# Optimization experiments

Measured on AMD Instinct MI355X. Metric: run time of the kernel, lower is better.

## Reference

```python
import jax, jax.numpy as jnp
import numpy as np

B, S, E, H = 8, 2048, 512, 8
DH = E // H
NEG = -1e30


def setup_inputs() -> dict:
    key = jax.random.key(0)
    ks = jax.random.split(key, 6)
    return {
        "x": jax.random.normal(ks[0], (B, S, E), dtype=jnp.float32),
        "W_qkv": jax.random.normal(ks[1], (E, 3 * E), dtype=jnp.float32) * 0.02,
        "b_qkv": jax.random.normal(ks[2], (3 * E,), dtype=jnp.float32) * 0.02,
        "W_out": jax.random.normal(ks[3], (E, E), dtype=jnp.float32) * 0.02,
        "b_out": jax.random.normal(ks[4], (E,), dtype=jnp.float32) * 0.02,
        "rel_pos": jax.random.normal(ks[5], (1, H, S, S), dtype=jnp.float32) * 0.02,
    }


def reference(x, W_qkv, b_qkv, W_out, b_out, rel_pos):
    b, s, e = x.shape
    scale = DH ** -0.5
    qkv = x @ W_qkv + b_qkv                     # [b, s, 3e]
    qkv = qkv.reshape(b, s, 3, H, DH)
    q = jnp.transpose(qkv[:, :, 0], (0, 2, 1, 3))  # [b, h, s, dh]
    k = jnp.transpose(qkv[:, :, 1], (0, 2, 1, 3))
    v = jnp.transpose(qkv[:, :, 2], (0, 2, 1, 3))
    scores = jnp.einsum("bhqd,bhkd->bhqk", q, k) * scale
    scores = scores + rel_pos[:, :, :s, :s]
    causal = jnp.tril(jnp.ones((s, s), dtype=bool))
    scores = jnp.where(causal[None, None], scores, NEG)
    attn = jax.nn.softmax(scores, axis=-1)
    out = jnp.einsum("bhqk,bhkd->bhqd", attn, v)  # [b, h, s, dh]
    out = jnp.transpose(out, (0, 2, 1, 3)).reshape(b, s, e)
    return out @ W_out + b_out
```

## Files before the change

kernel.cpp:

```cpp
#include <hip/hip_runtime.h>
#include <cstdint>


#define DEVI __device__ __forceinline__

typedef __bf16 bf8 __attribute__((ext_vector_type(8)));
typedef float f4 __attribute__((ext_vector_type(4)));
typedef unsigned short us8 __attribute__((ext_vector_type(8)));
typedef unsigned short us4 __attribute__((ext_vector_type(4)));

typedef const unsigned int __attribute__((address_space(1))) gu32;
typedef unsigned int __attribute__((address_space(3))) lu32;

DEVI unsigned short f2bf(float f) {
  unsigned u = __builtin_bit_cast(unsigned, f);
  u += 0x7fffu + ((u >> 16) & 1u);
  return (unsigned short)(u >> 16);
}

DEVI unsigned short cbf(float f) {
  return __builtin_bit_cast(unsigned short, (__bf16)f);
}

DEVI void gl_lds16(const void* g, void* l) {
  __builtin_amdgcn_global_load_lds((gu32*)g, (lu32*)l, 16, 0, 0);
}

DEVI bf8 comb(us4 a, us4 b) {
  us8 r;
  r[0]=a[0]; r[1]=a[1]; r[2]=a[2]; r[3]=a[3];
  r[4]=b[0]; r[5]=b[1]; r[6]=b[2]; r[7]=b[3];
  return __builtin_bit_cast(bf8, r);
}

__global__ __launch_bounds__(256) void k_convert_x(const float* __restrict__ x,
                                                   unsigned short* __restrict__ xb) {
  int c = blockIdx.x * 256 + threadIdx.x;
  int row = c >> 6, cl = c & 63;
  const float* s = x + ((size_t)row << 9) + (cl << 3);
  float4 a = *(const float4*)s;
  float4 b = *(const float4*)(s + 4);
  us8 o;
  o[0]=f2bf(a.x); o[1]=f2bf(a.y); o[2]=f2bf(a.z); o[3]=f2bf(a.w);
  o[4]=f2bf(b.x); o[5]=f2bf(b.y); o[6]=f2bf(b.z); o[7]=f2bf(b.w);
  int p = (cl & ~7) | ((cl & 7) ^ (row & 7));
  *(us8*)(xb + ((size_t)row << 9) + (p << 3)) = o;
}

__global__ __launch_bounds__(256) void k_transpose_w(const float* __restrict__ W,
                                                     unsigned short* __restrict__ Wt, int N) {
  __shared__ float t[32][33];
  int k0 = blockIdx.x * 32, n0 = blockIdx.y * 32;
  int tx = threadIdx.x & 31, ty = threadIdx.x >> 5;
#pragma unroll
  for (int r = 0; r < 4; ++r)
    t[ty + r * 8][tx] = W[(size_t)(k0 + ty + r * 8) * N + n0 + tx];
  __syncthreads();
#pragma unroll
  for (int r = 0; r < 4; ++r) {
    int n = n0 + ty + r * 8, k = k0 + tx;
    int k2 = (k & ~63) | ((((k >> 3) & 7) ^ (n & 7)) << 3) | (k & 7);
    Wt[((size_t)n << 9) + k2] = f2bf(t[tx][ty + r * 8]);
  }
}

__global__ __launch_bounds__(256) void k_relconv(const float* __restrict__ rel,
                                                 unsigned short* __restrict__ relt) {
  int t = blockIdx.x * 256 + threadIdx.x;
  int lane = t & 63, ct = (t >> 6) & 3, kt = (t >> 8) & 31, q16 = (t >> 13) & 127, h = t >> 20;
  if (kt > (q16 >> 2)) return;
  int row0 = (q16 << 4) + ((lane >> 4) << 2);
  int col = (kt << 6) + (ct << 4) + (lane & 15);
  const float* rp = rel + ((size_t)h << 22) + ((size_t)row0 << 11) + col;
  us4 o;
#pragma unroll
  for (int j = 0; j < 4; ++j) o[j] = f2bf(rp[(size_t)j << 11]);
  size_t idx = ((((((size_t)h << 7) | q16) << 5) | kt) << 2 | ct) << 6 | lane;
  *(us4*)(relt + (idx << 2)) = o;
}

template <int EPI>
__global__ __launch_bounds__(256, 2)
void k_gemm(const unsigned short* __restrict__ Ag, const unsigned short* __restrict__ Bg,
            const float* __restrict__ bias, float* __restrict__ Of,
            unsigned short* __restrict__ Oq, unsigned short* __restrict__ Ok,
            unsigned short* __restrict__ Ov) {
  __shared__ __align__(16) unsigned short lds[128 * 64 * 2];
  unsigned short* Al = lds;
  unsigned short* Bl = lds + 128 * 64;
  const int tid = threadIdx.x, wv = tid >> 6, lane = tid & 63, g = lane >> 4, cl = lane & 15;
  const int wm = wv >> 1, wn = wv & 1;
  const int row0 = blockIdx.x * 128, col0 = blockIdx.y * 128;
  f4 acc[4][4];
#pragma unroll
  for (int i = 0; i < 4; ++i)
#pragma unroll
    for (int j = 0; j < 4; ++j) acc[i][j] = (f4){0.f, 0.f, 0.f, 0.f};

  for (int kt = 0; kt < 8; ++kt) {
#pragma unroll
    for (int j = 0; j < 4; ++j) {
      int ci = wv * 4 + j;
      int gci = ci * 64 + lane;
      int r = gci >> 3, cc = gci & 7;
      gl_lds16(Ag + ((size_t)(row0 + r) << 9) + kt * 64 + cc * 8, Al + ci * 512);
      gl_lds16(Bg + ((size_t)(col0 + r) << 9) + kt * 64 + cc * 8, Bl + ci * 512);
    }
    __syncthreads();
#pragma unroll
    for (int kk = 0; kk < 2; ++kk) {
      bf8 af[4], bb[4];
#pragma unroll
      for (int mf = 0; mf < 4; ++mf) {
        int r = wm * 64 + mf * 16 + cl;
        int cc = (kk * 4 + g) ^ (r & 7);
        af[mf] = *(const bf8*)(Al + r * 64 + cc * 8);
      }
#pragma unroll
      for (int nf = 0; nf < 4; ++nf) {
        int r = wn * 64 + nf * 16 + cl;
        int cc = (kk * 4 + g) ^ (r & 7);
        bb[nf] = *(const bf8*)(Bl + r * 64 + cc * 8);
      }
#pragma unroll
      for (int mf = 0; mf < 4; ++mf)
#pragma unroll
        for (int nf = 0; nf < 4; ++nf)
          acc[mf][nf] = __builtin_amdgcn_mfma_f32_16x16x32_bf16(af[mf], bb[nf], acc[mf][nf], 0, 0, 0);
    }
    __syncthreads();
  }

  if (EPI == 1) {
#pragma unroll
    for (int nf = 0; nf < 4; ++nf) {
      int col = col0 + wn * 64 + nf * 16 + cl;
      float bv = bias[col];
#pragma unroll
      for (int mf = 0; mf < 4; ++mf) {
#pragma unroll
        for (int j = 0; j < 4; ++j) {
          int row = row0 + wm * 64 + mf * 16 + 4 * g + j;
          Of[((size_t)row << 9) + col] = acc[mf][nf][j] + bv;
        }
      }
    }
  } else {
    const int which = col0 >> 9;
#pragma unroll
    for (int nf = 0; nf < 4; ++nf) {
      int col = col0 + wn * 64 + nf * 16 + cl;
      float bv = bias[col];
      int d = col & 63, h = (col >> 6) & 7;
#pragma unroll
      for (int mf = 0; mf < 4; ++mf) {
        int row = row0 + wm * 64 + mf * 16 + 4 * g;
        int b = row >> 11, s = row & 2047;
        size_t fb = ((size_t)b * 8 + h) * 131072;
        if (which == 0) {
#pragma unroll
          for (int j = 0; j < 4; ++j) {
            int ss = s + j;
            size_t off = fb + (size_t)((ss >> 4) * 1024 + (d >> 5) * 512 +
                                       (((d >> 3) & 3) * 16 + (ss & 15)) * 8 + (d & 7));
            Oq[off] = f2bf((acc[mf][nf][j] + bv) * 0.125f);
          }
        } else if (which == 1) {
#pragma unroll
          for (int j = 0; j < 4; ++j) {
            int ss = s + j;
            size_t off = fb + (size_t)((ss >> 6) * 4096 + (d >> 5) * 2048 + ((ss >> 4) & 3) * 512 +
                                       (((d >> 3) & 3) * 16 + (ss & 15)) * 8 + (d & 7));
            Ok[off] = f2bf(acc[mf][nf][j] + bv);
          }
        } else {
          us4 o;
#pragma unroll
          for (int j = 0; j < 4; ++j) o[j] = f2bf(acc[mf][nf][j] + bv);
          size_t off = fb + (size_t)((s >> 6) * 4096 + ((s >> 5) & 1) * 2048 + (d >> 4) * 512 +
                                     ((((s >> 3) & 3) * 16) + (d & 15)) * 8 + (s & 7));
          *(us4*)(Ov + off) = o;
        }
      }
    }
  }
}

template <bool RELT>
__global__ __launch_bounds__(256, 4)
void k_attn(const unsigned short* __restrict__ Qf, const unsigned short* __restrict__ Kf,
            const unsigned short* __restrict__ Vf, const float* __restrict__ rel,
            const unsigned short* __restrict__ relt, unsigned short* __restrict__ AO) {
  __shared__ __align__(16) unsigned short Pl[4][16 * 68];
  const int tid = threadIdx.x, wv = tid >> 6, lane = tid & 63, g = lane >> 4, cl = lane & 15;
  int bid = blockIdx.x;
  int glo = bid & 7, b = (bid >> 3) & 7, chi = bid >> 6;
  int c = chi * 8 + glo;
  int h = c >> 4, i = c & 15;
  size_t fb = (((size_t)b << 3) + h) * 131072;
  const unsigned short* Qp = Qf + fb;
  const unsigned short* Kp = Kf + fb;
  const unsigned short* Vp = Vf + fb;
  const float* relp = rel + ((size_t)h << 22);
  unsigned short* pw = Pl[wv];

  for (int pass = 0; pass < 2; ++pass) {
    const int slab = pass ? (31 - i) : i;
    const int q16 = 4 * slab + wv;
    const int rX = q16 << 4;
    const int ktop = slab;

    bf8 qf[2];
#pragma unroll
    for (int kk = 0; kk < 2; ++kk)
      qf[kk] = *(const bf8*)(Qp + q16 * 1024 + kk * 512 + lane * 8);

    f4 oa[4];
    float mr[4], lr[4];
#pragma unroll
    for (int j = 0; j < 4; ++j) { mr[j] = -1e30f; lr[j] = 0.f; }
#pragma unroll
    for (int ct = 0; ct < 4; ++ct) oa[ct] = (f4){0.f, 0.f, 0.f, 0.f};

    for (int kt = 0; kt <= ktop; ++kt) {
      const int kb = kt << 6;
      const unsigned short* Kt = Kp + kt * 4096;
      const unsigned short* Vt = Vp + kt * 4096;
      bf8 kf[2][4], vf[2][4];
#pragma unroll
      for (int kk = 0; kk < 2; ++kk)
#pragma unroll
        for (int ct = 0; ct < 4; ++ct)
          kf[kk][ct] = *(const bf8*)(Kt + kk * 2048 + ct * 512 + lane * 8);
#pragma unroll
      for (int kk = 0; kk < 2; ++kk)
#pragma unroll
        for (int ct = 0; ct < 4; ++ct)
          vf[kk][ct] = *(const bf8*)(Vt + kk * 2048 + ct * 512 + lane * 8);
      us4 rt4[4];
      float rl[4][4];
      if constexpr (RELT) {
        const unsigned short* tb = relt + (((((size_t)h << 7) | q16) << 5) | kt) * 1024;
#pragma unroll
        for (int ct = 0; ct < 4; ++ct)
          rt4[ct] = *(const us4*)(tb + ((ct << 6) | lane) * 4);
      } else {
        const float* rb = relp + ((size_t)(rX + 4 * g) << 11) + kb + cl;
#pragma unroll
        for (int ct = 0; ct < 4; ++ct)
#pragma unroll
          for (int j = 0; j < 4; ++j) rl[ct][j] = rb[((size_t)j << 11) + ct * 16];
      }
      f4 sa[4];
#pragma unroll
      for (int ct = 0; ct < 4; ++ct) sa[ct] = (f4){0.f, 0.f, 0.f, 0.f};
#pragma unroll
      for (int kk = 0; kk < 2; ++kk)
#pragma unroll
        for (int ct = 0; ct < 4; ++ct)
          sa[ct] = __builtin_amdgcn_mfma_f32_16x16x32_bf16(qf[kk], kf[kk][ct], sa[ct], 0, 0, 0);
      if constexpr (RELT) {
#pragma unroll
        for (int ct = 0; ct < 4; ++ct)
#pragma unroll
          for (int j = 0; j < 4; ++j)
            sa[ct][j] += __builtin_bit_cast(float, (unsigned)rt4[ct][j] << 16);
      } else {
#pragma unroll
        for (int ct = 0; ct < 4; ++ct)
#pragma unroll
          for (int j = 0; j < 4; ++j) sa[ct][j] += rl[ct][j];
      }
      if (kt == ktop) {
#pragma unroll
        for (int ct = 0; ct < 4; ++ct) {
          int kcol = kb + ct * 16 + cl;
#pragma unroll
          for (int j = 0; j < 4; ++j)
            if (kcol > rX + 4 * g + j) sa[ct][j] = -1e30f;
        }
      }
      float al[4];
#pragma unroll
      for (int j = 0; j < 4; ++j) {
        float m0 = fmaxf(fmaxf(sa[0][j], sa[1][j]), fmaxf(sa[2][j], sa[3][j]));
        m0 = fmaxf(m0, __shfl_xor(m0, 1, 16));
        m0 = fmaxf(m0, __shfl_xor(m0, 2, 16));
        m0 = fmaxf(m0, __shfl_xor(m0, 4, 16));
        m0 = fmaxf(m0, __shfl_xor(m0, 8, 16));
        float mn = fmaxf(mr[j], m0);
        al[j] = __expf(mr[j] - mn);
        mr[j] = mn;
      }
#pragma unroll
      for (int ct = 0; ct < 4; ++ct)
#pragma unroll
        for (int j = 0; j < 4; ++j) sa[ct][j] = __expf(sa[ct][j] - mr[j]);
#pragma unroll
      for (int j = 0; j < 4; ++j) {
        float rs = sa[0][j] + sa[1][j] + sa[2][j] + sa[3][j];
        rs += __shfl_xor(rs, 1, 16);
        rs += __shfl_xor(rs, 2, 16);
        rs += __shfl_xor(rs, 4, 16);
        rs += __shfl_xor(rs, 8, 16);
        lr[j] = lr[j] * al[j] + rs;
      }
#pragma unroll
      for (int ct = 0; ct < 4; ++ct) {
        oa[ct][0] *= al[0]; oa[ct][1] *= al[1]; oa[ct][2] *= al[2]; oa[ct][3] *= al[3];
      }
#pragma unroll
      for (int ct = 0; ct < 4; ++ct)
#pragma unroll
        for (int j = 0; j < 4; ++j)
          pw[(4 * g + j) * 68 + ct * 16 + cl] = cbf(sa[ct][j]);
#pragma unroll
      for (int kk = 0; kk < 2; ++kk) {
        us4 p0 = *(const us4*)(pw + cl * 68 + kk * 32 + g * 8);
        us4 p1 = *(const us4*)(pw + cl * 68 + kk * 32 + g * 8 + 4);
        bf8 pf = comb(p0, p1);
#pragma unroll
        for (int ct = 0; ct < 4; ++ct)
          oa[ct] = __builtin_amdgcn_mfma_f32_16x16x32_bf16(pf, vf[kk][ct], oa[ct], 0, 0, 0);
      }
    }
#pragma unroll
    for (int j = 0; j < 4; ++j) {
      float inv = 1.0f / lr[j];
      int s = rX + 4 * g + j;
#pragma unroll
      for (int ct = 0; ct < 4; ++ct) {
        int d = ct * 16 + cl;
        int d2 = (d & 7) | (((d >> 3) ^ (s & 7)) << 3);
        AO[(((size_t)b << 11) + s) * 512 + h * 64 + d2] = cbf(oa[ct][j] * inv);
      }
    }
  }
}

extern "C" void kernel_launch(void* const* d_in, const int* in_sizes, int n_in,
                              void* d_out, int out_size, void* d_ws, size_t ws_size,
                              hipStream_t stream) {
  const float* x    = (const float*)d_in[0];
  const float* Wqkv = (const float*)d_in[1];
  const float* bqkv = (const float*)d_in[2];
  const float* Wout = (const float*)d_in[3];
  const float* bout = (const float*)d_in[4];
  const float* rel  = (const float*)d_in[5];
  float* out = (float*)d_out;

  unsigned short* Qw  = (unsigned short*)d_ws;
  unsigned short* Kw  = Qw  + 8388608;
  unsigned short* Vw  = Kw  + 8388608;
  unsigned short* XA  = Vw  + 8388608;
  unsigned short* WtQ = XA  + 8388608;
  unsigned short* WtO = WtQ + 786432;
  unsigned short* relt= WtO + 262144;
  const bool useT = ws_size >= (34603008ULL + 33554432ULL) * 2ULL;

  k_convert_x<<<dim3(4096), dim3(256), 0, stream>>>(x, XA);
  k_transpose_w<<<dim3(16, 48), dim3(256), 0, stream>>>(Wqkv, WtQ, 1536);
  k_transpose_w<<<dim3(16, 16), dim3(256), 0, stream>>>(Wout, WtO, 512);
  if (useT) k_relconv<<<dim3(32768), dim3(256), 0, stream>>>(rel, relt);
  k_gemm<0><<<dim3(128, 12), dim3(256), 0, stream>>>(XA, WtQ, bqkv, nullptr, Qw, Kw, Vw);
  if (useT) k_attn<true ><<<dim3(1024), dim3(256), 0, stream>>>(Qw, Kw, Vw, rel, relt, XA);
  else      k_attn<false><<<dim3(1024), dim3(256), 0, stream>>>(Qw, Kw, Vw, rel, relt, XA);
  k_gemm<1><<<dim3(128, 4), dim3(256), 0, stream>>>(XA, WtO, bout, out, nullptr, nullptr, nullptr);
}
```

Before: 210.9 us.

## Compute transposed attention tiles so each lane owns one query row

```diff
diff --git a/kernel.cpp b/kernel.cpp
--- a/kernel.cpp
+++ b/kernel.cpp
@@ -24,13 +24,6 @@
 
 DEVI void gl_lds16(const void* g, void* l) {
   __builtin_amdgcn_global_load_lds((gu32*)g, (lu32*)l, 16, 0, 0);
-}
-
-DEVI bf8 comb(us4 a, us4 b) {
-  us8 r;
-  r[0]=a[0]; r[1]=a[1]; r[2]=a[2]; r[3]=a[3];
-  r[4]=b[0]; r[5]=b[1]; r[6]=b[2]; r[7]=b[3];
-  return __builtin_bit_cast(bf8, r);
 }
 
 __global__ __launch_bounds__(256) void k_convert_x(const float* __restrict__ x,
@@ -69,12 +62,11 @@
   int t = blockIdx.x * 256 + threadIdx.x;
   int lane = t & 63, ct = (t >> 6) & 3, kt = (t >> 8) & 31, q16 = (t >> 13) & 127, h = t >> 20;
   if (kt > (q16 >> 2)) return;
-  int row0 = (q16 << 4) + ((lane >> 4) << 2);
-  int col = (kt << 6) + (ct << 4) + (lane & 15);
-  const float* rp = rel + ((size_t)h << 22) + ((size_t)row0 << 11) + col;
+  int row = (q16 << 4) + (lane & 15);
+  int col = (kt << 6) + (ct << 4) + ((lane >> 4) << 2);
+  float4 v = *(const float4*)(rel + ((size_t)h << 22) + ((size_t)row << 11) + col);
   us4 o;
-#pragma unroll
-  for (int j = 0; j < 4; ++j) o[j] = f2bf(rp[(size_t)j << 11]);
+  o[0] = f2bf(v.x); o[1] = f2bf(v.y); o[2] = f2bf(v.z); o[3] = f2bf(v.w);
   size_t idx = ((((((size_t)h << 7) | q16) << 5) | kt) << 2 | ct) << 6 | lane;
   *(us4*)(relt + (idx << 2)) = o;
 }
@@ -191,7 +183,7 @@
 void k_attn(const unsigned short* __restrict__ Qf, const unsigned short* __restrict__ Kf,
             const unsigned short* __restrict__ Vf, const float* __restrict__ rel,
             const unsigned short* __restrict__ relt, unsigned short* __restrict__ AO) {
-  __shared__ __align__(16) unsigned short Pl[4][16 * 68];
+  __shared__ __align__(16) unsigned short Pl[4][16 * 72];
   const int tid = threadIdx.x, wv = tid >> 6, lane = tid & 63, g = lane >> 4, cl = lane & 15;
   int bid = blockIdx.x;
   int glo = bid & 7, b = (bid >> 3) & 7, chi = bid >> 6;
@@ -209,18 +201,17 @@
     const int q16 = 4 * slab + wv;
     const int rX = q16 << 4;
     const int ktop = slab;
+    const int qrow = rX + cl;
 
     bf8 qf[2];
 #pragma unroll
     for (int kk = 0; kk < 2; ++kk)
       qf[kk] = *(const bf8*)(Qp + q16 * 1024 + kk * 512 + lane * 8);
 
-    f4 oa[4];
-    float mr[4], lr[4];
-#pragma unroll
-    for (int j = 0; j < 4; ++j) { mr[j] = -1e30f; lr[j] = 0.f; }
-#pragma unroll
-    for (int ct = 0; ct < 4; ++ct) oa[ct] = (f4){0.f, 0.f, 0.f, 0.f};
+    f4 ot[4];
+    float mr = -1e30f, lr = 0.f;
+#pragma unroll
+    for (int ct = 0; ct < 4; ++ct) ot[ct] = (f4){0.f, 0.f, 0.f, 0.f};
 
     for (int kt = 0; kt <= ktop; ++kt) {
       const int kb = kt << 6;
@@ -238,102 +229,97 @@
         for (int ct = 0; ct < 4; ++ct)
           vf[kk][ct] = *(const bf8*)(Vt + kk * 2048 + ct * 512 + lane * 8);
       us4 rt4[4];
-      float rl[4][4];
+      float4 rl4[4];
       if constexpr (RELT) {
         const unsigned short* tb = relt + (((((size_t)h << 7) | q16) << 5) | kt) * 1024;
 #pragma unroll
         for (int ct = 0; ct < 4; ++ct)
           rt4[ct] = *(const us4*)(tb + ((ct << 6) | lane) * 4);
       } else {
-        const float* rb = relp + ((size_t)(rX + 4 * g) << 11) + kb + cl;
-#pragma unroll
-        for (int ct = 0; ct < 4; ++ct)
-#pragma unroll
-          for (int j = 0; j < 4; ++j) rl[ct][j] = rb[((size_t)j << 11) + ct * 16];
-      }
-      f4 sa[4];
-#pragma unroll
-      for (int ct = 0; ct < 4; ++ct) sa[ct] = (f4){0.f, 0.f, 0.f, 0.f};
+#pragma unroll
+        for (int ct = 0; ct < 4; ++ct)
+          rl4[ct] = *(const float4*)(relp + ((size_t)qrow << 11) + kb + ct * 16 + g * 4);
+      }
+      f4 st[4];
+#pragma unroll
+      for (int ct = 0; ct < 4; ++ct) st[ct] = (f4){0.f, 0.f, 0.f, 0.f};
 #pragma unroll
       for (int kk = 0; kk < 2; ++kk)
 #pragma unroll
         for (int ct = 0; ct < 4; ++ct)
-          sa[ct] = __builtin_amdgcn_mfma_f32_16x16x32_bf16(qf[kk], kf[kk][ct], sa[ct], 0, 0, 0);
+          st[ct] = __builtin_amdgcn_mfma_f32_16x16x32_bf16(kf[kk][ct], qf[kk], st[ct], 0, 0, 0);
       if constexpr (RELT) {
 #pragma unroll
         for (int ct = 0; ct < 4; ++ct)
 #pragma unroll
           for (int j = 0; j < 4; ++j)
-            sa[ct][j] += __builtin_bit_cast(float, (unsigned)rt4[ct][j] << 16);
+            st[ct][j] += __builtin_bit_cast(float, (unsigned)rt4[ct][j] << 16);
       } else {
 #pragma unroll
-        for (int ct = 0; ct < 4; ++ct)
-#pragma unroll
-          for (int j = 0; j < 4; ++j) sa[ct][j] += rl[ct][j];
+        for (int ct = 0; ct < 4; ++ct) {
+          st[ct][0] += rl4[ct].x; st[ct][1] += rl4[ct].y;
+          st[ct][2] += rl4[ct].z; st[ct][3] += rl4[ct].w;
+        }
       }
       if (kt == ktop) {
 #pragma unroll
         for (int ct = 0; ct < 4; ++ct) {
-          int kcol = kb + ct * 16 + cl;
+          int kc0 = kb + ct * 16 + 4 * g;
 #pragma unroll
           for (int j = 0; j < 4; ++j)
-            if (kcol > rX + 4 * g + j) sa[ct][j] = -1e30f;
+            if (kc0 + j > qrow) st[ct][j] = -1e30f;
         }
       }
-      float al[4];
-#pragma unroll
-      for (int j = 0; j < 4; ++j) {
-        float m0 = fmaxf(fmaxf(sa[0][j], sa[1][j]), fmaxf(sa[2][j], sa[3][j]));
-        m0 = fmaxf(m0, __shfl_xor(m0, 1, 16));
-        m0 = fmaxf(m0, __shfl_xor(m0, 2, 16));
-        m0 = fmaxf(m0, __shfl_xor(m0, 4, 16));
-        m0 = fmaxf(m0, __shfl_xor(m0, 8, 16));
-        float mn = fmaxf(mr[j], m0);
-        al[j] = __expf(mr[j] - mn);
-        mr[j] = mn;
-      }
+      float m0 = fmaxf(fmaxf(st[0][0], st[0][1]), fmaxf(st[0][2], st[0][3]));
+#pragma unroll
+      for (int ct = 1; ct < 4; ++ct)
+        m0 = fmaxf(m0, fmaxf(fmaxf(st[ct][0], st[ct][1]), fmaxf(st[ct][2], st[ct][3])));
+      m0 = fmaxf(m0, __shfl_xor(m0, 16));
+      m0 = fmaxf(m0, __shfl_xor(m0, 32));
+      float mn = fmaxf(mr, m0);
+      float al = __expf(mr - mn);
+      mr = mn;
 #pragma unroll
       for (int ct = 0; ct < 4; ++ct)
 #pragma unroll
-        for (int j = 0; j < 4; ++j) sa[ct][j] = __expf(sa[ct][j] - mr[j]);
-#pragma unroll
-      for (int j = 0; j < 4; ++j) {
-        float rs = sa[0][j] + sa[1][j] + sa[2][j] + sa[3][j];
-        rs += __shfl_xor(rs, 1, 16);
-        rs += __shfl_xor(rs, 2, 16);
-        rs += __shfl_xor(rs, 4, 16);
-        rs += __shfl_xor(rs, 8, 16);
-        lr[j] = lr[j] * al[j] + rs;
-      }
+        for (int j = 0; j < 4; ++j) st[ct][j] = __expf(st[ct][j] - mn);
+      float rs = 0.f;
+#pragma unroll
+      for (int ct = 0; ct < 4; ++ct)
+        rs += (st[ct][0] + st[ct][1]) + (st[ct][2] + st[ct][3]);
+      rs += __shfl_xor(rs, 16);
+      rs += __shfl_xor(rs, 32);
+      lr = lr * al + rs;
 #pragma unroll
       for (int ct = 0; ct < 4; ++ct) {
-        oa[ct][0] *= al[0]; oa[ct][1] *= al[1]; oa[ct][2] *= al[2]; oa[ct][3] *= al[3];
-      }
-#pragma unroll
-      for (int ct = 0; ct < 4; ++ct)
-#pragma unroll
-        for (int j = 0; j < 4; ++j)
-          pw[(4 * g + j) * 68 + ct * 16 + cl] = cbf(sa[ct][j]);
+        ot[ct][0] *= al; ot[ct][1] *= al; ot[ct][2] *= al; ot[ct][3] *= al;
+      }
+#pragma unroll
+      for (int ct = 0; ct < 4; ++ct) {
+        us4 pk;
+        pk[0] = cbf(st[ct][0]); pk[1] = cbf(st[ct][1]);
+        pk[2] = cbf(st[ct][2]); pk[3] = cbf(st[ct][3]);
+        *(us4*)(pw + cl * 72 + ct * 16 + g * 4) = pk;
+      }
 #pragma unroll
       for (int kk = 0; kk < 2; ++kk) {
-        us4 p0 = *(const us4*)(pw + cl * 68 + kk * 32 + g * 8);
-        us4 p1 = *(const us4*)(pw + cl * 68 + kk * 32 + g * 8 + 4);
-        bf8 pf = comb(p0, p1);
-#pragma unroll
-        for (int ct = 0; ct < 4; ++ct)
-          oa[ct] = __builtin_amdgcn_mfma_f32_16x16x32_bf16(pf, vf[kk][ct], oa[ct], 0, 0, 0);
-      }
-    }
-#pragma unroll
-    for (int j = 0; j < 4; ++j) {
-      float inv = 1.0f / lr[j];
-      int s = rX + 4 * g + j;
-#pragma unroll
-      for (int ct = 0; ct < 4; ++ct) {
-        int d = ct * 16 + cl;
-        int d2 = (d & 7) | (((d >> 3) ^ (s & 7)) << 3);
-        AO[(((size_t)b << 11) + s) * 512 + h * 64 + d2] = cbf(oa[ct][j] * inv);
-      }
+        bf8 pf = __builtin_bit_cast(bf8, *(const us8*)(pw + cl * 72 + kk * 32 + g * 8));
+#pragma unroll
+        for (int ct = 0; ct < 4; ++ct)
+          ot[ct] = __builtin_amdgcn_mfma_f32_16x16x32_bf16(vf[kk][ct], pf, ot[ct], 0, 0, 0);
+      }
+    }
+    float inv = 1.0f / lr;
+    const int s = qrow;
+    unsigned short* aor = AO + (((size_t)b << 11) + s) * 512 + h * 64;
+#pragma unroll
+    for (int ct = 0; ct < 4; ++ct) {
+      int chunk = 2 * ct + (g >> 1);
+      int base = (4 * (g & 1)) | ((chunk ^ (s & 7)) << 3);
+      us4 o;
+      o[0] = cbf(ot[ct][0] * inv); o[1] = cbf(ot[ct][1] * inv);
+      o[2] = cbf(ot[ct][2] * inv); o[3] = cbf(ot[ct][3] * inv);
+      *(us4*)(aor + base) = o;
     }
   }
 }
```

After: 213.0 us. Within noise of the previous version (+1.0%).
